# Performance work log

Hardware: AMD Instinct MI355X
Metric: run time of the kernel (lower is better)

## Reference

```python
import jax, jax.numpy as jnp
import numpy as np

M = 128  # template / canvas size (hardcoded in the module)


def _pair_indices(nodes_per_image):
    # Static (host-side) ragged pair construction, mirroring the Python loop
    # in the torch forward. Returns compressed index arrays for valid pairs.
    npi = np.asarray(nodes_per_image)
    idx_a, idx_b, batch, valid = [], [], [], []
    off = 0
    for b, n in enumerate(npi.tolist()):
        a = np.repeat(np.arange(n), n) + off   # repeat_interleave
        c = np.tile(np.arange(n), n) + off     # .repeat(n, 1)
        idx_a.append(a); idx_b.append(c)
        batch.append(np.full(n * n, b))
        if n > 1:
            v = np.triu(np.ones((n, n)), 1).astype(bool).reshape(-1)
        else:
            v = np.zeros((n * n,), bool)
        valid.append(v)
        off += n
    return (np.concatenate(idx_a), np.concatenate(idx_b),
            np.concatenate(batch), np.concatenate(valid))


def _grid_sample_bilinear(img, gx, gy):
    # img [O, M, M]; gx, gy [O, H, W] in [-1, 1]; align_corners=True, zero padding
    ix = (gx + 1.0) * 0.5 * (M - 1)
    iy = (gy + 1.0) * 0.5 * (M - 1)
    x0 = jnp.floor(ix); y0 = jnp.floor(iy)
    wx = ix - x0; wy = iy - y0
    out = jnp.zeros_like(gx)
    corners = ((0, 0, (1 - wy) * (1 - wx)), (0, 1, (1 - wy) * wx),
               (1, 0, wy * (1 - wx)), (1, 1, wy * wx))
    for dy, dx, w in corners:
        xi = x0 + dx; yi = y0 + dy
        inb = (xi >= 0) & (xi <= M - 1) & (yi >= 0) & (yi <= M - 1)
        xc = jnp.clip(xi, 0, M - 1).astype(jnp.int32)
        yc = jnp.clip(yi, 0, M - 1).astype(jnp.int32)
        v = jax.vmap(lambda m, yy, xx: m[yy, xx])(img, yc, xc)
        out = out + w * jnp.where(inb, v, 0.0)
    return out


def masks_to_layout(vecs, boxes, masks, obj_to_img, num_images, H):
    # sg2im-style: warp each mask into its box, scale by vec, scatter-add per image
    x0 = boxes[:, 0][:, None, None]; y0 = boxes[:, 1][:, None, None]
    x1 = boxes[:, 2][:, None, None]; y1 = boxes[:, 3][:, None, None]
    X = jnp.linspace(0.0, 1.0, H)[None, None, :]   # [1,1,W]
    Y = jnp.linspace(0.0, 1.0, H)[None, :, None]   # [1,H,1]
    gx = ((X - x0) / (x1 - x0)) * 2.0 - 1.0        # [O,1,W]
    gy = ((Y - y0) / (y1 - y0)) * 2.0 - 1.0        # [O,H,1]
    O = boxes.shape[0]
    gx = jnp.broadcast_to(gx, (O, H, H))
    gy = jnp.broadcast_to(gy, (O, H, H))
    sampled = _grid_sample_bilinear(masks, gx, gy)           # [O,H,W]
    sampled = sampled * vecs[:, 0][:, None, None]            # D = 1 channel
    out = jax.ops.segment_sum(sampled, obj_to_img, num_segments=num_images)
    return out[:, None]  # [B,1,H,W] (segment_sum already zero-pads empty images)


def _forward(nodes, adj_mat, nodes_per_image):
    ii = jnp.arange(M)
    # eye(128) max-pooled with k=11, s=1, p=5 -> band of half-width 10
    line_template = (jnp.abs(ii[:, None] - ii[None, :]) <= 10).astype(jnp.float32)
    idx_a, idx_b, batch_ids, valid = _pair_indices(nodes_per_image)
    sel = np.nonzero(valid)[0]
    idx_a = idx_a[sel]; idx_b = idx_b[sel]
    obj_to_img = jnp.asarray(batch_ids[sel], dtype=jnp.int32)
    boxes = jnp.concatenate([nodes[idx_a], nodes[idx_b]], axis=1)  # [O,4]
    vecs = adj_mat[sel]                                            # [O,1]
    B = int(np.asarray(nodes_per_image).shape[0])
    dual_slope = (jnp.abs((boxes[:, 3] - boxes[:, 1]) / (jnp.abs(boxes[:, 2] - boxes[:, 0]) + 1e-6))
                  + jnp.abs((boxes[:, 2] - boxes[:, 0]) / (jnp.abs(boxes[:, 3] - boxes[:, 1]) + 1e-6)))
    t = jnp.clip(2.0 * jax.nn.sigmoid(0.03 * (dual_slope - 2.0)) - 1.0, 0.0, 1.0)
    t = t[:, None, None]
    masks = (1.0 - t) * line_template[None, :, :] + t  # rect_template == ones
    img = masks_to_layout(vecs, boxes, masks, obj_to_img, B, M)
    return jnp.clip(img, 0.0, 1.0)


def setup_inputs() -> dict:
    key = jax.random.key(0)
    k1, k2 = jax.random.split(key)
    B, n = 24, 16
    nodes = jax.random.uniform(k1, (B * n, 2), dtype=jnp.float32)       # [384,2] in [0,1]
    adj_mat = jax.random.uniform(k2, (B * n * n, 1), dtype=jnp.float32)  # [6144,1]
    nodes_per_image = np.full((B,), n, dtype=np.int64)  # static ragged sizes
    return {"nodes": nodes, "adj_mat": adj_mat, "nodes_per_image": nodes_per_image}


def reference(nodes, adj_mat, nodes_per_image):
    return _forward(nodes, adj_mat, nodes_per_image)
```

## Files before the change

kernel.cpp:

```cpp
#include <hip/hip_runtime.h>

#define MM    128
#define NN    16
#define NPAIR 120
#define NIMG  24
#define ROWS_PER_BLK 2
#define BLOCKS_PER_IMG 64

__global__ __launch_bounds__(256) void g2i_kernel(
    const float* __restrict__ nodes,
    const float* __restrict__ adj,
    float* __restrict__ out)
{
    __shared__ float2 s_ab[NPAIR];
    __shared__ float2 s_xi[NPAIR];
    __shared__ float4 s_row[NPAIR * ROWS_PER_BLK];
    __shared__ int    s_cnt;

    const int img = blockIdx.x >> 6;
    const int blk = blockIdx.x & 63;
    const int r0  = blk * ROWS_PER_BLK;
    const int tid = threadIdx.x;

    if (tid == 0) s_cnt = 0;
    __syncthreads();

    if (tid < NPAIR) {
        int k = tid, i = 0;
        while (k >= (NN - 1 - i)) { k -= (NN - 1 - i); ++i; }
        const int j = i + 1 + k;
        const float x0 = nodes[(img * NN + i) * 2 + 0];
        const float y0 = nodes[(img * NN + i) * 2 + 1];
        const float x1 = nodes[(img * NN + j) * 2 + 0];
        const float y1 = nodes[(img * NN + j) * 2 + 1];
        const float dx = x1 - x0, dy = y1 - y0;

        const float ya  = 127.0f * y0 - dy;
        const float yb  = 127.0f * y0 + 128.0f * dy;
        const float ylo = fminf(ya, yb) - 0.5f;
        const float yhi = fmaxf(ya, yb) + 0.5f;

        if (yhi >= (float)r0 && ylo <= (float)(r0 + ROWS_PER_BLK - 1)) {
            const float ds = fabsf(dy) / (fabsf(dx) + 1e-6f)
                           + fabsf(dx) / (fabsf(dy) + 1e-6f);
            float t = 2.0f / (1.0f + expf(-0.03f * (ds - 2.0f))) - 1.0f;
            t = fminf(fmaxf(t, 0.0f), 1.0f);
            const float vec = adj[img * NN * NN + i * NN + j];
            const float p = vec * t;
            const float q = vec * (1.0f - t);

            const float xa = 127.0f * x0 - dx;
            const float xb = 127.0f * x0 + 128.0f * dx;

            const int slot = atomicAdd(&s_cnt, 1);
            s_ab[slot] = make_float2(1.0f / dx, -127.0f * x0 / dx);
            s_xi[slot] = make_float2(fminf(xa, xb) - 0.5f, fmaxf(xa, xb) + 0.5f);

            const float cay = 1.0f / dy;
            const float cby = -127.0f * y0 / dy;
            #pragma unroll
            for (int r = 0; r < ROWS_PER_BLK; ++r) {
                const float iy  = (float)(r0 + r) * cay + cby;
                const float y0f = floorf(iy);
                const float wy  = iy - y0f;
                const float ey0 = (y0f >=  0.0f && y0f <= 127.0f) ? (1.0f - wy) : 0.0f;
                const float ey1 = (y0f >= -1.0f && y0f <= 126.0f) ? wy          : 0.0f;
                s_row[slot * ROWS_PER_BLK + r] =
                    make_float4(q * ey0, q * ey1, p * (ey0 + ey1), y0f);
            }
        }
    }
    __syncthreads();
    const int cnt = s_cnt;

    const int w    = tid >> 6;
    const int lane = tid & 63;
    const int px   = w * 32 + (lane & 31);
    const int row  = lane >> 5;
    const int py   = r0 + row;
    const float fx  = (float)px;
    const float wlo = (float)(w * 32) - 0.5f;
    const float whi = (float)(w * 32) + 31.5f;

    float acc = 0.0f;

    for (int s = 0; s < cnt; ++s) {
        const float2 xi = s_xi[s];
        if (xi.y < wlo || xi.x > whi) continue;

        const float2 ab = s_ab[s];
        const float4 ry = s_row[s * ROWS_PER_BLK + row];

        const float ix  = fmaf(fx, ab.x, ab.y);
        const float x0f = floorf(ix);
        const float wx  = ix - x0f;
        const float ex0 = (x0f >=  0.0f && x0f <= 127.0f) ? (1.0f - wx) : 0.0f;
        const float ex1 = (x0f >= -1.0f && x0f <= 126.0f) ? wx          : 0.0f;

        const float df  = ry.w - x0f;
        const float l00 = (fabsf(df)        <= 10.0f) ? 1.0f : 0.0f;
        const float l01 = (fabsf(df - 1.0f) <= 10.0f) ? 1.0f : 0.0f;
        const float l10 = (fabsf(df + 1.0f) <= 10.0f) ? 1.0f : 0.0f;

        acc = fmaf(ry.z, ex0 + ex1, acc);
        acc = fmaf(ry.x, fmaf(ex0, l00, ex1 * l01), acc);
        acc = fmaf(ry.y, fmaf(ex0, l10, ex1 * l00), acc);
    }

    acc = fminf(fmaxf(acc, 0.0f), 1.0f);
    out[(size_t)img * (MM * MM) + py * MM + px] = acc;
}

extern "C" void kernel_launch(void* const* d_in, const int* in_sizes, int n_in,
                              void* d_out, int out_size, void* d_ws, size_t ws_size,
                              hipStream_t stream) {
    const float* nodes = (const float*)d_in[0];
    const float* adj   = (const float*)d_in[1];
    float* out = (float*)d_out;
    g2i_kernel<<<dim3(NIMG * BLOCKS_PER_IMG), dim3(256), 0, stream>>>(nodes, adj, out);
}
```

Baseline: 73.60 us.

## Bin line segments per 32-column window and prefetch next entry from LDS

Each segment is now appended to a per-window list in shared memory for each of the four 32-pixel column windows it overlaps. This replaces the single list that every wave scanned with a per-entry x-range test. Each wave iterates only its own window's list and software-prefetches the next entry, removing the skip branch and divergence. Strip order is also permuted across images to spread the load. The cost is more shared memory, more atomics in setup, and a one-past-end prefetch read that CAP=121 covers.

Result: faster. 69.15 us (-6.0%).

```diff
diff --git a/kernel.cpp b/kernel.cpp
--- a/kernel.cpp
+++ b/kernel.cpp
@@ -5,24 +5,25 @@
 #define NPAIR 120
 #define NIMG  24
 #define ROWS_PER_BLK 2
-#define BLOCKS_PER_IMG 64
+#define STRIPS 64
+#define NWIN   4
+#define CAP    121
 
 __global__ __launch_bounds__(256) void g2i_kernel(
     const float* __restrict__ nodes,
     const float* __restrict__ adj,
     float* __restrict__ out)
 {
-    __shared__ float2 s_ab[NPAIR];
-    __shared__ float2 s_xi[NPAIR];
-    __shared__ float4 s_row[NPAIR * ROWS_PER_BLK];
-    __shared__ int    s_cnt;
+    __shared__ float2 s_ab [NWIN][CAP];
+    __shared__ float4 s_row[NWIN][CAP * ROWS_PER_BLK];
+    __shared__ int    s_cnt[NWIN];
 
-    const int img = blockIdx.x >> 6;
-    const int blk = blockIdx.x & 63;
-    const int r0  = blk * ROWS_PER_BLK;
-    const int tid = threadIdx.x;
+    const int img   = blockIdx.x >> 6;
+    const int strip = (((blockIdx.x & 63) * 21) + img * 7) & 63;
+    const int r0    = strip * ROWS_PER_BLK;
+    const int tid   = threadIdx.x;
 
-    if (tid == 0) s_cnt = 0;
+    if (tid < NWIN) s_cnt[tid] = 0;
     __syncthreads();
 
     if (tid < NPAIR) {
@@ -49,15 +50,9 @@
             const float p = vec * t;
             const float q = vec * (1.0f - t);
 
-            const float xa = 127.0f * x0 - dx;
-            const float xb = 127.0f * x0 + 128.0f * dx;
-
-            const int slot = atomicAdd(&s_cnt, 1);
-            s_ab[slot] = make_float2(1.0f / dx, -127.0f * x0 / dx);
-            s_xi[slot] = make_float2(fminf(xa, xb) - 0.5f, fmaxf(xa, xb) + 0.5f);
-
             const float cay = 1.0f / dy;
             const float cby = -127.0f * y0 / dy;
+            float4 rd[ROWS_PER_BLK];
             #pragma unroll
             for (int r = 0; r < ROWS_PER_BLK; ++r) {
                 const float iy  = (float)(r0 + r) * cay + cby;
@@ -65,31 +60,47 @@
                 const float wy  = iy - y0f;
                 const float ey0 = (y0f >=  0.0f && y0f <= 127.0f) ? (1.0f - wy) : 0.0f;
                 const float ey1 = (y0f >= -1.0f && y0f <= 126.0f) ? wy          : 0.0f;
-                s_row[slot * ROWS_PER_BLK + r] =
-                    make_float4(q * ey0, q * ey1, p * (ey0 + ey1), y0f);
+                rd[r] = make_float4(q * ey0, q * ey1, p * (ey0 + ey1), y0f);
+            }
+
+            const float2 ab = make_float2(1.0f / dx, -127.0f * x0 / dx);
+            const float xa  = 127.0f * x0 - dx;
+            const float xb  = 127.0f * x0 + 128.0f * dx;
+            const float xlo = fminf(xa, xb) - 0.5f;
+            const float xhi = fmaxf(xa, xb) + 0.5f;
+
+            #pragma unroll
+            for (int w = 0; w < NWIN; ++w) {
+                const float wl = (float)(w * 32) - 0.5f;
+                const float wh = (float)(w * 32) + 31.5f;
+                if (xhi >= wl && xlo <= wh) {
+                    const int slot = atomicAdd(&s_cnt[w], 1);
+                    s_ab [w][slot] = ab;
+                    s_row[w][slot * ROWS_PER_BLK + 0] = rd[0];
+                    s_row[w][slot * ROWS_PER_BLK + 1] = rd[1];
+                }
             }
         }
     }
     __syncthreads();
-    const int cnt = s_cnt;
 
     const int w    = tid >> 6;
     const int lane = tid & 63;
-    const int px   = w * 32 + (lane & 31);
+    const int px   = (w << 5) + (lane & 31);
     const int row  = lane >> 5;
     const int py   = r0 + row;
-    const float fx  = (float)px;
-    const float wlo = (float)(w * 32) - 0.5f;
-    const float whi = (float)(w * 32) + 31.5f;
+    const float fx = (float)px;
+    const int  cnt = s_cnt[w];
 
     float acc = 0.0f;
+    float2 ab_n = s_ab[w][0];
+    float4 ry_n = s_row[w][row];
 
     for (int s = 0; s < cnt; ++s) {
-        const float2 xi = s_xi[s];
-        if (xi.y < wlo || xi.x > whi) continue;
-
-        const float2 ab = s_ab[s];
-        const float4 ry = s_row[s * ROWS_PER_BLK + row];
+        const float2 ab = ab_n;
+        const float4 ry = ry_n;
+        ab_n = s_ab[w][s + 1];
+        ry_n = s_row[w][(s + 1) * ROWS_PER_BLK + row];
 
         const float ix  = fmaf(fx, ab.x, ab.y);
         const float x0f = floorf(ix);
@@ -117,5 +128,5 @@
     const float* nodes = (const float*)d_in[0];
     const float* adj   = (const float*)d_in[1];
     float* out = (float*)d_out;
-    g2i_kernel<<<dim3(NIMG * BLOCKS_PER_IMG), dim3(256), 0, stream>>>(nodes, adj, out);
+    g2i_kernel<<<dim3(NIMG * STRIPS), dim3(256), 0, stream>>>(nodes, adj, out);
 }
```
